# Performance work log

Hardware: AMD Instinct MI355X
Metric: run time of the kernel (lower is better)

Reference implementation:

```python
import jax, jax.numpy as jnp
import numpy as np

SCALE = 0.0625      # spatial_scale
OUT = 7             # out_size (== part_size)
C_OUT = 256         # output_dim (== input channels, group_size=1)
SPP = 4             # sample_per_part
TRANS_STD = 0.1
FC_DIM = 1024
B, H, W = 4, 128, 128
N_ROI = 2000
IMG = 2048.0        # H / SCALE


def _round_half(x):
    # CUDA round(): half away from zero (coords are non-negative here)
    return jnp.floor(x + 0.5)


def deform_roi_pool(data, rois, offset):
    """Faithful port of deform_roi_pooling (DCNv2 deform PS-ROI pooling, group_size=1).
    data: [B,C,H,W]; rois: [N,5]; offset: None or [N,2,OUT,OUT]. Returns [N,C,OUT,OUT]."""
    Bn, C, Hh, Ww = data.shape
    N = rois.shape[0]
    b = rois[:, 0].astype(jnp.int32)
    sw = _round_half(rois[:, 1]) * SCALE - 0.5
    sh = _round_half(rois[:, 2]) * SCALE - 0.5
    ew = (_round_half(rois[:, 3]) + 1.0) * SCALE - 0.5
    eh = (_round_half(rois[:, 4]) + 1.0) * SCALE - 0.5
    rw = jnp.maximum(ew - sw, 0.1)
    rh = jnp.maximum(eh - sh, 0.1)
    bw, bh = rw / OUT, rh / OUT              # bin sizes
    subw, subh = bw / SPP, bh / SPP          # sub-bin sizes

    ph, pw = jnp.meshgrid(jnp.arange(OUT, dtype=data.dtype),
                          jnp.arange(OUT, dtype=data.dtype), indexing='ij')
    wstart = pw[None] * bw[:, None, None] + sw[:, None, None]   # [N,OUT,OUT]
    hstart = ph[None] * bh[:, None, None] + sh[:, None, None]
    if offset is not None:
        # part_size == out_size -> part index == bin index
        wstart = wstart + offset[:, 0] * TRANS_STD * rw[:, None, None]
        hstart = hstart + offset[:, 1] * TRANS_STD * rh[:, None, None]

    ih2, iw2 = jnp.meshgrid(jnp.arange(SPP, dtype=data.dtype),
                            jnp.arange(SPP, dtype=data.dtype), indexing='ij')
    ih2, iw2 = ih2.reshape(-1), iw2.reshape(-1)  # [SPP*SPP]
    # sample coords [S2, N, OUT, OUT]
    ws = wstart[None] + iw2[:, None, None, None] * subw[None, :, None, None]
    hs = hstart[None] + ih2[:, None, None, None] * subh[None, :, None, None]

    bb = b[:, None, None]  # [N,1,1]

    def body(carry, coords):
        acc, cnt = carry
        w, h = coords                                 # [N,OUT,OUT]
        valid = (w >= -0.5) & (w <= Ww - 0.5) & (h >= -0.5) & (h <= Hh - 0.5)
        wc = jnp.clip(w, 0.0, Ww - 1.0)
        hc = jnp.clip(h, 0.0, Hh - 1.0)
        x0 = jnp.floor(wc).astype(jnp.int32)
        y0 = jnp.floor(hc).astype(jnp.int32)
        x1 = jnp.minimum(x0 + 1, Ww - 1)
        y1 = jnp.minimum(y0 + 1, Hh - 1)
        dx = wc - x0
        dy = hc - y0
        v00 = data[bb, :, y0, x0]   # [N,OUT,OUT,C]
        v01 = data[bb, :, y0, x1]
        v10 = data[bb, :, y1, x0]
        v11 = data[bb, :, y1, x1]
        val = (((1 - dx) * (1 - dy))[..., None] * v00
               + (dx * (1 - dy))[..., None] * v01
               + ((1 - dx) * dy)[..., None] * v10
               + (dx * dy)[..., None] * v11)
        val = jnp.where(valid[..., None], val, 0.0)
        return (acc + val, cnt + valid.astype(data.dtype)), None

    init = (jnp.zeros((N, OUT, OUT, C), data.dtype),
            jnp.zeros((N, OUT, OUT), data.dtype))
    (s, cnt), _ = jax.lax.scan(body, init, (ws, hs))
    out = jnp.where(cnt[..., None] > 0, s / jnp.maximum(cnt, 1.0)[..., None], 0.0)
    return jnp.transpose(out, (0, 3, 1, 2))  # [N,C,OUT,OUT]


def setup_inputs() -> dict:
    key = jax.random.key(0)
    ks = jax.random.split(key, 16)
    data = jax.random.normal(ks[0], (B, C_OUT, H, W), dtype=jnp.float32)
    bidx = jax.random.randint(ks[1], (N_ROI,), 0, B).astype(jnp.float32)
    x1 = jax.random.uniform(ks[2], (N_ROI,), minval=0.0, maxval=IMG - 64.0)
    y1 = jax.random.uniform(ks[3], (N_ROI,), minval=0.0, maxval=IMG - 64.0)
    wbox = jax.random.uniform(ks[4], (N_ROI,), minval=16.0, maxval=400.0)
    hbox = jax.random.uniform(ks[5], (N_ROI,), minval=16.0, maxval=400.0)
    rois = jnp.stack([bidx, x1, y1,
                      jnp.minimum(x1 + wbox, IMG - 1.0),
                      jnp.minimum(y1 + hbox, IMG - 1.0)], axis=1)
    fin = OUT * OUT * C_OUT  # 12544
    def lin(k, i, o, s=None):
        s = (1.0 / np.sqrt(i)) if s is None else s
        return jax.random.normal(k, (i, o), dtype=jnp.float32) * s
    return {
        'data': data, 'rois': rois,
        'w1': lin(ks[6], fin, FC_DIM), 'b1': jnp.zeros((FC_DIM,), jnp.float32),
        'w2': lin(ks[7], FC_DIM, FC_DIM), 'b2': jnp.zeros((FC_DIM,), jnp.float32),
        'w3': lin(ks[8], FC_DIM, OUT * OUT * 2, 0.01), 'b3': jnp.zeros((OUT * OUT * 2,), jnp.float32),
        'mw1': lin(ks[9], fin, FC_DIM), 'mb1': jnp.zeros((FC_DIM,), jnp.float32),
        'mw2': lin(ks[10], FC_DIM, OUT * OUT, 0.01), 'mb2': jnp.zeros((OUT * OUT,), jnp.float32),
    }


def reference(data, rois, w1, b1, w2, b2, w3, b3, mw1, mb1, mw2, mb2):
    n = rois.shape[0]
    x = deform_roi_pool(data, rois, None)              # [N,C,OUT,OUT]
    xf = x.reshape(n, -1)
    h = jax.nn.relu(xf @ w1 + b1)
    h = jax.nn.relu(h @ w2 + b2)
    offset = (h @ w3 + b3).reshape(n, 2, OUT, OUT)
    m = jax.nn.relu(xf @ mw1 + mb1)
    mask = jax.nn.sigmoid(m @ mw2 + mb2).reshape(n, 1, OUT, OUT)
    feat = deform_roi_pool(data, rois, offset) * mask
    return feat
```

## Files before the change

kernel.cpp:

```cpp
#include <hip/hip_runtime.h>
#include <math.h>

#define WDIM 128
#define HDIM 128
#define BDIM 4
#define CDIM 256
#define NROI 2000
#define MPAD 2048
#define FIN  12544
#define FC   1024
#define HWC  (HDIM * WDIM * CDIM)

typedef unsigned short bf16r;
typedef unsigned short u16;
typedef __attribute__((ext_vector_type(8))) short bf16x8;
typedef __attribute__((ext_vector_type(4))) float f32x4;
typedef __attribute__((ext_vector_type(8))) _Float16 half8;
typedef __attribute__((ext_vector_type(8))) unsigned short ushort8v;

__device__ __forceinline__ bf16r f2bf(float f) {
    unsigned u = __float_as_uint(f);
    u += 0x7FFFu + ((u >> 16) & 1u);
    return (bf16r)(u >> 16);
}
__device__ __forceinline__ float bf2f(bf16r h) {
    return __uint_as_float(((unsigned)h) << 16);
}
__device__ __forceinline__ u16 f2h(float f) {
    union { u16 s; _Float16 h; } c; c.h = (_Float16)f; return c.s;
}

__device__ __forceinline__ void async16(const bf16r* g, bf16r* l) {
    __builtin_amdgcn_global_load_lds(
        (const __attribute__((address_space(1))) unsigned int*)g,
        (__attribute__((address_space(3))) unsigned int*)l, 16, 0, 0);
}

#define VMW(n) asm volatile("s_waitcnt vmcnt(" #n ")" ::: "memory")
#define BARRIER() __builtin_amdgcn_s_barrier()

__device__ __forceinline__ void roi_geom(const float* __restrict__ rois, int n,
                                         int& b, float& sw, float& sh,
                                         float& rw, float& rh) {
    const float* r = rois + (size_t)n * 5;
    b = (int)r[0];
    float r1 = floorf(r[1] + 0.5f);
    float r2 = floorf(r[2] + 0.5f);
    float r3 = floorf(r[3] + 0.5f);
    float r4 = floorf(r[4] + 0.5f);
    sw = r1 * 0.0625f - 0.5f;
    sh = r2 * 0.0625f - 0.5f;
    float ew = (r3 + 1.0f) * 0.0625f - 0.5f;
    float eh = (r4 + 1.0f) * 0.0625f - 0.5f;
    rw = fmaxf(ew - sw, 0.1f);
    rh = fmaxf(eh - sh, 0.1f);
}

__device__ __forceinline__ void build_geometry(
        int n, int tid, const float* __restrict__ rois,
        const float* __restrict__ offs,
        const float* __restrict__ maskb,
        float* axW, unsigned* axMeta, uint2* wpix, int* npx, float* scale) {
    if (tid < 98) {
        int po = tid >> 1, axis = tid & 1;
        int b; float sw, sh, rw, rh;
        roi_geom(rois, n, b, sw, sh, rw, rh);
        float bw = rw * (1.f / 7.f), bh = rh * (1.f / 7.f);
        int ph = po / 7, pw = po - ph * 7;
        float start, sub;
        if (axis == 0) {
            start = (float)pw * bw + sw;
            if (offs) start += offs[(size_t)n * 98 + po] * 0.1f * rw;
            sub = bw * 0.25f;
        } else {
            start = (float)ph * bh + sh;
            if (offs) start += offs[(size_t)n * 98 + 49 + po] * 0.1f * rh;
            sub = bh * 0.25f;
        }
        float wsl[5] = {0.f, 0.f, 0.f, 0.f, 0.f};
        int base = 0, cnt = 0, mx = 0, any = 0;
#pragma unroll
        for (int i = 0; i < 4; ++i) {
            float p = start + (float)i * sub;
            bool valid = (p >= -0.5f) & (p <= 127.5f);
            float pc = fminf(fmaxf(p, 0.f), 127.f);
            int p0 = (int)floorf(pc);
            float d = pc - (float)p0;
            int p1 = min(p0 + 1, 127);
            if (valid) {
                if (!any) { base = p0; any = 1; }
                int c0 = p0 - base, c1 = p1 - base;
                float w0 = 1.f - d;
#pragma unroll
                for (int k = 0; k < 5; ++k)
                    wsl[k] += ((c0 == k) ? w0 : 0.f) + ((c1 == k) ? d : 0.f);
                cnt++;
                mx = max(mx, c1);
            }
        }
        int N = any ? mx + 1 : 0;
        axMeta[tid] = (unsigned)(N | (cnt << 3) | (base << 6));
#pragma unroll
        for (int k = 0; k < 5; ++k) axW[tid * 5 + k] = wsl[k];
    }
    __syncthreads();
    if (tid < 245) {
        int po = tid / 5, r = tid - po * 5;
        unsigned mx_ = axMeta[po * 2], my_ = axMeta[po * 2 + 1];
        int NX = mx_ & 7, NY = my_ & 7;
        int bx = (mx_ >> 6) & 127, by = (my_ >> 6) & 127;
        if (r == 0) {
            int cntx = (mx_ >> 3) & 7, cnty = (my_ >> 3) & 7;
            int ct = cntx * cnty;
            float sc = (ct > 0) ? 1.f / (float)ct : 0.f;
            if (maskb) sc *= (ct > 0) ? maskb[(size_t)n * 49 + po] : 0.f;
            npx[po] = NX * NY;
            scale[po] = sc;
        }
        if (r < NY) {
            float wyr = axW[(po * 2 + 1) * 5 + r];
            unsigned rowoff = (unsigned)(((by + r) * 128 + bx) * 512);
#pragma unroll
            for (int c = 0; c < 5; ++c)
                if (c < NX)
                    wpix[po * 28 + r * NX + c] =
                        make_uint2(rowoff + (unsigned)c * 512u,
                                   __float_as_uint(wyr * axW[po * 2 * 5 + c]));
        }
    }
    __syncthreads();
}

__device__ __forceinline__ void conv_body(const float* __restrict__ srcA,
                                          const float* __restrict__ srcB,
                                          int nsplit, int ncols, int Nout, int K,
                                          int kb, int nb, bf16r* __restrict__ dst,
                                          float (*t)[33], int tid) {
    int k0 = kb << 5, n0 = nb << 5;
    int tx = tid & 31, ty = tid >> 5;
#pragma unroll
    for (int i = 0; i < 32; i += 8) {
        int k = k0 + ty + i;
        int n = n0 + tx;
        const float* s = (n < nsplit) ? srcA : srcB;
        int col = (n < nsplit) ? n : n - nsplit;
        float v = (n < Nout && col < ncols) ? s[(size_t)k * ncols + col] : 0.f;
        t[ty + i][tx] = v;
    }
    __syncthreads();
#pragma unroll
    for (int i = 0; i < 32; i += 8) {
        int n = n0 + ty + i;
        if (n < Nout) dst[(size_t)n * K + k0 + tx] = f2bf(t[tx][ty + i]);
    }
}

__global__ __launch_bounds__(256) void prep_kernel(
        const float* __restrict__ w1, const float* __restrict__ mw1,
        const float* __restrict__ w2, const float* __restrict__ w3,
        const float* __restrict__ mw2,
        bf16r* __restrict__ bt1, bf16r* __restrict__ bt2,
        bf16r* __restrict__ bt3, bf16r* __restrict__ bt4,
        const float* __restrict__ data, u16* __restrict__ data_t) {
    __shared__ float t[32][33];
    int tid = threadIdx.x;
    int blk = blockIdx.x;
    if (blk < 25088) {
        conv_body(w1, mw1, 1024, 1024, 2048, FIN, blk % 392, blk / 392, bt1, t, tid);
        return;
    }
    blk -= 25088;
    if (blk < 1024) {
        conv_body(w2, w2, 1 << 30, 1024, 1024, 1024, blk & 31, blk >> 5, bt2, t, tid);
        return;
    }
    blk -= 1024;
    if (blk < 128) {
        conv_body(w3, w3, 1 << 30, 98, 98, 1024, blk & 31, blk >> 5, bt3, t, tid);
        return;
    }
    blk -= 128;
    if (blk < 64) {
        conv_body(mw2, mw2, 1 << 30, 49, 49, 1024, blk & 31, blk >> 5, bt4, t, tid);
        return;
    }
    blk -= 64;
    {
        int x0 = (blk & 3) << 5;
        int c0 = ((blk >> 2) & 7) << 5;
        int bz = blk >> 5;
        int b = bz >> 7, y = bz & 127;
        int tx = tid & 31, ty = tid >> 5;
#pragma unroll
        for (int i = 0; i < 32; i += 8)
            t[ty + i][tx] = data[(((size_t)b * CDIM + c0 + ty + i) * HDIM + y) * WDIM + x0 + tx];
        __syncthreads();
#pragma unroll
        for (int i = 0; i < 32; i += 8)
            data_t[(((size_t)b * HDIM + y) * WDIM + x0 + ty + i) * CDIM + c0 + tx] = f2h(t[tx][ty + i]);
    }
}

__global__ __launch_bounds__(512) void pool1_kernel(const u16* __restrict__ data_t,
                                                    const float* __restrict__ rois,
                                                    bf16r* __restrict__ xf) {
    __shared__ ushort tileX[49][264];
    __shared__ float axW[98 * 5];
    __shared__ unsigned axMeta[98];
    __shared__ uint2 wpix[49 * 28];
    __shared__ int npx[49];
    __shared__ float scale[49];
    int n = blockIdx.x, tid = threadIdx.x;
    build_geometry(n, tid, rois, nullptr, nullptr, axW, axMeta, wpix, npx, scale);
    int b = (int)rois[(size_t)n * 5];
    int wave = tid >> 6, lane = tid & 63, shalf = lane >> 5, c8 = (lane & 31) << 3;
    const char* dpb = (const char*)(data_t + (size_t)b * HWC + c8);
    for (int po = wave * 2 + shalf; po < 49; po += 16) {
        int npe = npx[po];
        float sc = scale[po];
        const uint2* wp = wpix + po * 28;
        float a[8];
#pragma unroll
        for (int k = 0; k < 8; ++k) a[k] = 0.f;
        int p = 0;
        for (; p + 2 <= npe; p += 2) {
            uint2 q0 = wp[p], q1 = wp[p + 1];
            half8 v0 = *(const half8*)(dpb + q0.x);
            half8 v1 = *(const half8*)(dpb + q1.x);
            float w0 = __uint_as_float(q0.y), w1 = __uint_as_float(q1.y);
#pragma unroll
            for (int k = 0; k < 8; ++k) a[k] += w0 * (float)v0[k];
#pragma unroll
            for (int k = 0; k < 8; ++k) a[k] += w1 * (float)v1[k];
        }
        if (p < npe) {
            uint2 q0 = wp[p];
            half8 v0 = *(const half8*)(dpb + q0.x);
            float w0 = __uint_as_float(q0.y);
#pragma unroll
            for (int k = 0; k < 8; ++k) a[k] += w0 * (float)v0[k];
        }
        ushort8v o;
#pragma unroll
        for (int k = 0; k < 8; ++k) o[k] = f2bf(a[k] * sc);
        *(ushort8v*)&tileX[po][c8] = o;
    }
    __syncthreads();
    bf16r* xp = xf + (size_t)n * FIN;
    for (int u = tid; u < 3136; u += 512) {
        int k0 = u << 2;
        ushort4 o;
#pragma unroll
        for (int j = 0; j < 4; ++j) {
            int k = k0 + j;
            int c = k / 49;
            int po = k - c * 49;
            ((ushort*)&o)[j] = tileX[po][c];
        }
        *(ushort4*)(xp + k0) = o;
    }
}

__global__ __launch_bounds__(512) void pool2_kernel(const u16* __restrict__ data_t,
                                                    const float* __restrict__ rois,
                                                    const float* __restrict__ offs,
                                                    const float* __restrict__ maskb,
                                                    float* __restrict__ out) {
    __shared__ float tile[49 * 128];
    __shared__ float axW[98 * 5];
    __shared__ unsigned axMeta[98];
    __shared__ uint2 wpix[49 * 28];
    __shared__ int npx[49];
    __shared__ float scale[49];
    int n = blockIdx.x, chalf = blockIdx.y, tid = threadIdx.x;
    build_geometry(n, tid, rois, offs, maskb, axW, axMeta, wpix, npx, scale);
    int b = (int)rois[(size_t)n * 5];
    int wave = tid >> 6, lane = tid & 63, q = lane >> 4, c8 = (lane & 15) << 3;
    const char* dpb = (const char*)(data_t + (size_t)b * HWC + chalf * 128 + c8);
    for (int po = wave * 4 + q; po < 49; po += 32) {
        int npe = npx[po];
        float sc = scale[po];
        const uint2* wp = wpix + po * 28;
        float a[8];
#pragma unroll
        for (int k = 0; k < 8; ++k) a[k] = 0.f;
        int p = 0;
        for (; p + 2 <= npe; p += 2) {
            uint2 q0 = wp[p], q1 = wp[p + 1];
            half8 v0 = *(const half8*)(dpb + q0.x);
            half8 v1 = *(const half8*)(dpb + q1.x);
            float w0 = __uint_as_float(q0.y), w1 = __uint_as_float(q1.y);
#pragma unroll
            for (int k = 0; k < 8; ++k) a[k] += w0 * (float)v0[k];
#pragma unroll
            for (int k = 0; k < 8; ++k) a[k] += w1 * (float)v1[k];
        }
        if (p < npe) {
            uint2 q0 = wp[p];
            half8 v0 = *(const half8*)(dpb + q0.x);
            float w0 = __uint_as_float(q0.y);
#pragma unroll
            for (int k = 0; k < 8; ++k) a[k] += w0 * (float)v0[k];
        }
        int cs = c8 ^ ((po & 7) << 3);
        float4 lo = make_float4(a[0] * sc, a[1] * sc, a[2] * sc, a[3] * sc);
        float4 hi = make_float4(a[4] * sc, a[5] * sc, a[6] * sc, a[7] * sc);
        *(float4*)&tile[po * 128 + cs] = lo;
        *(float4*)&tile[po * 128 + cs + 4] = hi;
    }
    __syncthreads();
    float* op = out + (size_t)n * FIN + (size_t)chalf * 6272;
    for (int i = tid; i < 6272; i += 512) {
        int c = i / 49, po = i - c * 49;
        op[i] = tile[po * 128 + (c ^ ((po & 7) << 3))];
    }
}

#define STAGE_A(buf, h, kt) do { \
    async16(Abase + (size_t)(kt) * 64 + sAoff[h][0], &lds[buf][0][((h) * 128 + wave * 8) * 64]); \
    async16(Abase + (size_t)(kt) * 64 + sAoff[h][1], &lds[buf][0][((h) * 128 + 64 + wave * 8) * 64]); \
} while (0)
#define STAGE_B(buf, h, kt) do { \
    async16(Bbase + (size_t)(kt) * 64 + sBoff[h][0], &lds[buf][1][((h) * 128 + wave * 8) * 64]); \
    async16(Bbase + (size_t)(kt) * 64 + sBoff[h][1], &lds[buf][1][((h) * 128 + 64 + wave * 8) * 64]); \
} while (0)
#define LDA_HALF(buf, mh) do { \
    const char* Ar = (const char*)&lds[buf][0][0] + aQ + (mh) * 16384; \
    _Pragma("unroll") for (int i = 0; i < 4; ++i) \
        _Pragma("unroll") for (int ks = 0; ks < 2; ++ks) \
            aF[i][ks] = *(const bf16x8*)(Ar + i * 2048 + fRB[ks]); \
} while (0)
#define LDB_HALF(dst, buf, nh) do { \
    const char* Br = (const char*)&lds[buf][1][0] + bQ + (nh) * 16384; \
    _Pragma("unroll") for (int jf = 0; jf < 2; ++jf) \
        _Pragma("unroll") for (int ks = 0; ks < 2; ++ks) \
            dst[jf][ks] = *(const bf16x8*)(Br + jf * 2048 + fRB[ks]); \
} while (0)
#define MMA_Q(mh, nh, B) do { \
    __builtin_amdgcn_s_setprio(1); \
    _Pragma("unroll") for (int i = 0; i < 4; ++i) \
        _Pragma("unroll") for (int jf = 0; jf < 2; ++jf) \
            _Pragma("unroll") for (int ks = 0; ks < 2; ++ks) \
                acc[(mh) * 4 + i][(nh) * 2 + jf] = __builtin_amdgcn_mfma_f32_16x16x32_bf16( \
                    aF[i][ks], B[jf][ks], acc[(mh) * 4 + i][(nh) * 2 + jf], 0, 0, 0); \
    __builtin_amdgcn_s_setprio(0); \
} while (0)

__global__ __launch_bounds__(512, 2) void gemm256_kernel(
        const bf16r* __restrict__ A, int lda,
        const bf16r* __restrict__ Bt, int ldb,
        bf16r* __restrict__ P, int Npad, int KS, int ktiles) {
    __shared__ bf16r lds[2][2][256 * 64];
    int tid = threadIdx.x;
    int wave = tid >> 6, lane = tid & 63;
    int l15 = lane & 15, quad = lane >> 4;
    int wm = wave >> 2, wn = wave & 3;

    int idx = blockIdx.x + gridDim.x * blockIdx.y;
    int nid = (idx & 7) * ((gridDim.x * gridDim.y) >> 3) + (idx >> 3);
    int bx = nid % gridDim.x, by = nid / gridDim.x;
    int m0 = by << 8, n0 = bx << 8;
    int z = blockIdx.z;

    int sAoff[2][2], sBoff[2][2];
#pragma unroll
    for (int h = 0; h < 2; ++h)
#pragma unroll
        for (int j = 0; j < 2; ++j) {
            int slot = h * 128 + j * 64 + wave * 8 + (lane >> 3);
            int g = (lane & 7) ^ ((slot >> 1) & 7);
            int rowA = ((slot >> 6) & 1) * 128 + (slot >> 7) * 64 + (slot & 63);
            int colB = ((slot >> 5) & 3) * 64 + (slot >> 7) * 32 + (slot & 31);
            sAoff[h][j] = rowA * lda + g * 8;
            sBoff[h][j] = colB * ldb + g * 8;
        }
    const bf16r* Abase = A + (size_t)m0 * lda;
    const bf16r* Bbase = Bt + (size_t)n0 * ldb;

    int fRB[2];
#pragma unroll
    for (int ks = 0; ks < 2; ++ks)
        fRB[ks] = l15 * 128 + ((((ks << 2) + quad) ^ ((l15 >> 1) & 7)) << 4);
    int aQ = wm * 8192;
    int bQ = wn * 4096;

    f32x4 acc[8][4];
#pragma unroll
    for (int i = 0; i < 8; ++i)
#pragma unroll
        for (int j = 0; j < 4; ++j) acc[i][j] = (f32x4){0.f, 0.f, 0.f, 0.f};
    bf16x8 aF[4][2], bF0[2][2], bF1[2][2];

    int tb = ((ktiles * z) / KS) & ~1;
    int te = (z == KS - 1) ? ktiles : ((ktiles * (z + 1)) / KS) & ~1;
    int nit = (te - tb) >> 1;

    STAGE_A(0, 0, tb); STAGE_B(0, 0, tb); STAGE_A(0, 1, tb); STAGE_B(0, 1, tb);
    STAGE_A(1, 0, tb + 1); STAGE_B(1, 0, tb + 1);
    VMW(4);
    BARRIER();

    for (int it = 0; it < nit; ++it) {
        int t1 = tb + 2 * it + 1, nx0 = t1 + 1, nx1 = t1 + 2;
        bool last = (it == nit - 1);
        LDA_HALF(0, 0); LDB_HALF(bF0, 0, 0);
        STAGE_A(1, 1, t1);
        BARRIER();
        MMA_Q(0, 0, bF0);
        BARRIER();

        LDB_HALF(bF1, 0, 1);
        STAGE_B(1, 1, t1);
        BARRIER();
        MMA_Q(0, 1, bF1);
        BARRIER();

        LDA_HALF(0, 1);
        if (!last) STAGE_A(0, 0, nx0);
        BARRIER();
        MMA_Q(1, 1, bF1);
        BARRIER();

        if (!last) STAGE_B(0, 0, nx0);
        BARRIER();
        MMA_Q(1, 0, bF0);
        if (last) { VMW(0); } else { VMW(4); }
        BARRIER();

        LDA_HALF(1, 0); LDB_HALF(bF0, 1, 0);
        if (!last) STAGE_A(0, 1, nx0);
        BARRIER();
        MMA_Q(0, 0, bF0);
        BARRIER();

        LDB_HALF(bF1, 1, 1);
        if (!last) STAGE_B(0, 1, nx0);
        BARRIER();
        MMA_Q(0, 1, bF1);
        BARRIER();

        LDA_HALF(1, 1);
        if (!last) STAGE_A(1, 0, nx1);
        BARRIER();
        MMA_Q(1, 1, bF1);
        BARRIER();

        if (!last) STAGE_B(1, 0, nx1);
        BARRIER();
        MMA_Q(1, 0, bF0);
        if (!last) { VMW(4); }
        BARRIER();
    }

    bf16r* Pp = P + (size_t)z * MPAD * Npad;
#pragma unroll
    for (int I = 0; I < 8; ++I) {
        int row = m0 + wm * 128 + I * 16 + quad * 4;
#pragma unroll
        for (int J = 0; J < 4; ++J) {
            int col = n0 + wn * 64 + J * 16 + l15;
            bf16r* o = Pp + (size_t)row * Npad + col;
#pragma unroll
            for (int r = 0; r < 4; ++r) o[(size_t)r * Npad] = f2bf(acc[I][J][r]);
        }
    }
}

__global__ __launch_bounds__(256) void gemm_mfma_kernel(
        const bf16r* __restrict__ A, int lda,
        const bf16r* __restrict__ Bt, int K,
        float* __restrict__ P, int Npad, int KS) {
    __shared__ bf16r As[128 * 32];
    __shared__ bf16r Bs[128 * 32];
    int tid = threadIdx.x;
    int wave = tid >> 6, lane = tid & 63;
    int nwgxy = gridDim.x * gridDim.y;
    int idx = blockIdx.x + gridDim.x * blockIdx.y;
    int chunk = nwgxy >> 3;
    int nid = (idx & 7) * chunk + (idx >> 3);
    int bx = nid % gridDim.x, by = nid / gridDim.x;
    int m0 = by << 7, n0 = bx << 7;
    int z = blockIdx.z;

    int srow = lane >> 2;
    int kchunk = ((lane & 3) ^ ((lane >> 3) & 3)) << 3;
    const bf16r* aG0 = A + (size_t)(m0 + wave * 32 + srow) * lda + kchunk;
    const bf16r* aG1 = A + (size_t)(m0 + wave * 32 + 16 + srow) * lda + kchunk;
    const bf16r* bG0 = Bt + (size_t)(n0 + wave * 32 + srow) * K + kchunk;
    const bf16r* bG1 = Bt + (size_t)(n0 + wave * 32 + 16 + srow) * K + kchunk;
    bf16r* aL0 = As + wave * 1024;
    bf16r* aL1 = As + wave * 1024 + 512;
    bf16r* bL0 = Bs + wave * 1024;
    bf16r* bL1 = Bs + wave * 1024 + 512;

    int l15 = lane & 15, quad = lane >> 4;
    int wr = wave >> 1, wc = wave & 1;
    int psw = (quad ^ ((l15 >> 1) & 3)) << 3;
    int aoff[4], boff[4];
#pragma unroll
    for (int t = 0; t < 4; ++t) {
        aoff[t] = ((wr * 64 + t * 16 + l15) * 32 + psw) * 2;
        boff[t] = ((wc * 64 + t * 16 + l15) * 32 + psw) * 2;
    }

    f32x4 acc[4][4];
#pragma unroll
    for (int i = 0; i < 4; ++i)
#pragma unroll
        for (int j = 0; j < 4; ++j) acc[i][j] = (f32x4){0.f, 0.f, 0.f, 0.f};

    int iters = K >> 5;
    int i0 = (int)((long)iters * z / KS);
    int i1 = (int)((long)iters * (z + 1) / KS);

    {
        size_t k0 = (size_t)i0 << 5;
        async16(aG0 + k0, aL0); async16(aG1 + k0, aL1);
        async16(bG0 + k0, bL0); async16(bG1 + k0, bL1);
    }
    for (int it = i0; it < i1; ++it) {
        __syncthreads();
        bf16x8 af[4], bfv[4];
#pragma unroll
        for (int t = 0; t < 4; ++t) af[t] = *(const bf16x8*)((const char*)As + aoff[t]);
#pragma unroll
        for (int t = 0; t < 4; ++t) bfv[t] = *(const bf16x8*)((const char*)Bs + boff[t]);
        __syncthreads();
        if (it + 1 < i1) {
            size_t k0 = (size_t)(it + 1) << 5;
            async16(aG0 + k0, aL0); async16(aG1 + k0, aL1);
            async16(bG0 + k0, bL0); async16(bG1 + k0, bL1);
        }
#pragma unroll
        for (int i = 0; i < 4; ++i)
#pragma unroll
            for (int j = 0; j < 4; ++j)
                acc[i][j] = __builtin_amdgcn_mfma_f32_16x16x32_bf16(af[i], bfv[j], acc[i][j], 0, 0, 0);
    }

    float* Pp = P + (size_t)z * MPAD * Npad;
#pragma unroll
    for (int i = 0; i < 4; ++i) {
        int row = m0 + wr * 64 + i * 16 + quad * 4;
#pragma unroll
        for (int j = 0; j < 4; ++j) {
            int col = n0 + wc * 64 + j * 16 + l15;
            float* o = Pp + (size_t)row * Npad + col;
#pragma unroll
            for (int r = 0; r < 4; ++r) o[(size_t)r * Npad] = acc[i][j][r];
        }
    }
}

__global__ __launch_bounds__(256) void gemm_tail_kernel(
        const bf16r* __restrict__ A0, int lda0,
        const bf16r* __restrict__ A1, int lda1,
        const bf16r* __restrict__ Bt0, const bf16r* __restrict__ Bt1,
        float* __restrict__ P) {
    __shared__ bf16r As[128 * 32];
    __shared__ bf16r Bs[128 * 32];
    int tid = threadIdx.x;
    int wave = tid >> 6, lane = tid & 63;
    int prob = blockIdx.y >> 4;
    int m0 = (blockIdx.y & 15) << 7;
    const bf16r* A = prob ? A1 : A0;
    int lda = prob ? lda1 : lda0;
    const bf16r* Bt = prob ? Bt1 : Bt0;
    int z = blockIdx.z;
    const int K = 1024, KS = 8, Npad = 128;

    int srow = lane >> 2;
    int kchunk = ((lane & 3) ^ ((lane >> 3) & 3)) << 3;
    const bf16r* aG0 = A + (size_t)(m0 + wave * 32 + srow) * lda + kchunk;
    const bf16r* aG1 = A + (size_t)(m0 + wave * 32 + 16 + srow) * lda + kchunk;
    const bf16r* bG0 = Bt + (size_t)(wave * 32 + srow) * K + kchunk;
    const bf16r* bG1 = Bt + (size_t)(wave * 32 + 16 + srow) * K + kchunk;
    bf16r* aL0 = As + wave * 1024;
    bf16r* aL1 = As + wave * 1024 + 512;
    bf16r* bL0 = Bs + wave * 1024;
    bf16r* bL1 = Bs + wave * 1024 + 512;

    int l15 = lane & 15, quad = lane >> 4;
    int wr = wave >> 1, wc = wave & 1;
    int psw = (quad ^ ((l15 >> 1) & 3)) << 3;
    int aoff[4], boff[4];
#pragma unroll
    for (int t = 0; t < 4; ++t) {
        aoff[t] = ((wr * 64 + t * 16 + l15) * 32 + psw) * 2;
        boff[t] = ((wc * 64 + t * 16 + l15) * 32 + psw) * 2;
    }

    f32x4 acc[4][4];
#pragma unroll
    for (int i = 0; i < 4; ++i)
#pragma unroll
        for (int j = 0; j < 4; ++j) acc[i][j] = (f32x4){0.f, 0.f, 0.f, 0.f};

    int iters = K >> 5;
    int i0 = iters * z / KS;
    int i1 = iters * (z + 1) / KS;

    {
        size_t k0 = (size_t)i0 << 5;
        async16(aG0 + k0, aL0); async16(aG1 + k0, aL1);
        async16(bG0 + k0, bL0); async16(bG1 + k0, bL1);
    }
    for (int it = i0; it < i1; ++it) {
        __syncthreads();
        bf16x8 af[4], bfv[4];
#pragma unroll
        for (int t = 0; t < 4; ++t) af[t] = *(const bf16x8*)((const char*)As + aoff[t]);
#pragma unroll
        for (int t = 0; t < 4; ++t) bfv[t] = *(const bf16x8*)((const char*)Bs + boff[t]);
        __syncthreads();
        if (it + 1 < i1) {
            size_t k0 = (size_t)(it + 1) << 5;
            async16(aG0 + k0, aL0); async16(aG1 + k0, aL1);
            async16(bG0 + k0, bL0); async16(bG1 + k0, bL1);
        }
#pragma unroll
        for (int i = 0; i < 4; ++i)
#pragma unroll
            for (int j = 0; j < 4; ++j)
                acc[i][j] = __builtin_amdgcn_mfma_f32_16x16x32_bf16(af[i], bfv[j], acc[i][j], 0, 0, 0);
    }

    float* Pp = P + (size_t)(prob * 8 + z) * (MPAD * 128);
#pragma unroll
    for (int i = 0; i < 4; ++i) {
        int row = m0 + wr * 64 + i * 16 + quad * 4;
#pragma unroll
        for (int j = 0; j < 4; ++j) {
            int col = wc * 64 + j * 16 + l15;
            float* o = Pp + (size_t)row * Npad + col;
#pragma unroll
            for (int r = 0; r < 4; ++r) o[(size_t)r * Npad] = acc[i][j][r];
        }
    }
}

__global__ __launch_bounds__(256) void reduce_kernel(
        const void* __restrict__ Pv, int shift, int KS, int pbf16,
        const float* __restrict__ bias0, const float* __restrict__ bias1, int bsplit,
        void* __restrict__ Out, int ldo, int M, int Nreal, int outmode) {
    int idx = (blockIdx.x * 256 + threadIdx.x) << 2;
    int Npad = 1 << shift;
    int row = idx >> shift, col = idx & (Npad - 1);
    f32x4 s = (f32x4){0.f, 0.f, 0.f, 0.f};
    size_t plane = (size_t)MPAD << shift;
    if (pbf16) {
        const bf16r* P = (const bf16r*)Pv;
        for (int zz = 0; zz < KS; ++zz) {
            ushort4 u = *(const ushort4*)(P + (size_t)zz * plane + idx);
            s[0] += bf2f(u.x); s[1] += bf2f(u.y); s[2] += bf2f(u.z); s[3] += bf2f(u.w);
        }
    } else {
        const float* P = (const float*)Pv;
        for (int zz = 0; zz < KS; ++zz) s += *(const f32x4*)(P + (size_t)zz * plane + idx);
    }
    if (row < M) {
#pragma unroll
        for (int e = 0; e < 4; ++e) {
            int c = col + e;
            if (c < Nreal) {
                float b = (c < bsplit) ? bias0[c] : bias1[c - bsplit];
                float v = s[e] + b;
                if (outmode == 0) {
                    v = fmaxf(v, 0.f);
                    ((bf16r*)Out)[(size_t)row * ldo + c] = f2bf(v);
                } else {
                    if (outmode == 2) v = 1.f / (1.f + expf(-v));
                    ((float*)Out)[(size_t)row * ldo + c] = v;
                }
            }
        }
    }
}

__global__ __launch_bounds__(256) void reduce34_kernel(
        const float* __restrict__ P, const float* __restrict__ b3,
        const float* __restrict__ mb2, float* __restrict__ offs,
        float* __restrict__ maskb) {
    int blk = blockIdx.x;
    int prob = blk >> 8;
    int idx = ((blk & 255) * 256 + threadIdx.x) << 2;
    int row = idx >> 7, col = idx & 127;
    f32x4 s = (f32x4){0.f, 0.f, 0.f, 0.f};
    size_t plane = (size_t)MPAD * 128;
    const float* Pb = P + (size_t)(prob * 8) * plane;
    for (int zz = 0; zz < 8; ++zz) s += *(const f32x4*)(Pb + (size_t)zz * plane + idx);
    if (row < NROI) {
        if (prob == 0) {
#pragma unroll
            for (int e = 0; e < 4; ++e) {
                int c = col + e;
                if (c < 98) offs[(size_t)row * 98 + c] = s[e] + b3[c];
            }
        } else {
#pragma unroll
            for (int e = 0; e < 4; ++e) {
                int c = col + e;
                if (c < 49) maskb[(size_t)row * 49 + c] = 1.f / (1.f + expf(-(s[e] + mb2[c])));
            }
        }
    }
}

extern "C" void kernel_launch(void* const* d_in, const int* in_sizes, int n_in,
                              void* d_out, int out_size, void* d_ws, size_t ws_size,
                              hipStream_t stream) {
    const float* data = (const float*)d_in[0];
    const float* rois = (const float*)d_in[1];
    const float* w1   = (const float*)d_in[2];
    const float* b1   = (const float*)d_in[3];
    const float* w2   = (const float*)d_in[4];
    const float* b2   = (const float*)d_in[5];
    const float* w3   = (const float*)d_in[6];
    const float* b3   = (const float*)d_in[7];
    const float* mw1  = (const float*)d_in[8];
    const float* mb1  = (const float*)d_in[9];
    const float* mw2  = (const float*)d_in[10];
    const float* mb2  = (const float*)d_in[11];
    float* out = (float*)d_out;

    char* w = (char*)d_ws;
    size_t off = 0;
    auto carve = [&](size_t bytes) {
        void* p = w + off;
        off += (bytes + 255) & ~(size_t)255;
        return p;
    };
    u16* data_t   = (u16*)carve((size_t)BDIM * HDIM * WDIM * CDIM * 2);
    bf16r* xf     = (bf16r*)carve((size_t)MPAD * FIN * 2);
    bf16r* bt1    = (bf16r*)carve((size_t)MPAD * FIN * 2);
    bf16r* hm     = (bf16r*)carve((size_t)MPAD * 2048 * 2);
    bf16r* h2     = (bf16r*)carve((size_t)MPAD * 1024 * 2);
    bf16r* bt2    = (bf16r*)carve((size_t)1024 * 1024 * 2);
    bf16r* bt3    = (bf16r*)carve((size_t)128 * 1024 * 2);
    bf16r* bt4    = (bf16r*)carve((size_t)128 * 1024 * 2);
    float* offs   = (float*)carve((size_t)NROI * 98 * 4);
    float* maskb  = (float*)carve((size_t)NROI * 49 * 4);
    void*  P      = (void*)(w + off);
    size_t plane  = (size_t)MPAD * 2048 * 4;
    size_t avail  = (ws_size > off) ? ws_size - off : 0;
    int use256 = (avail >= 4 * plane);

    prep_kernel<<<42688, 256, 0, stream>>>(w1, mw1, w2, w3, mw2,
                                           bt1, bt2, bt3, bt4, data, data_t);
    pool1_kernel<<<dim3(NROI), 512, 0, stream>>>(data_t, rois, xf);

    if (use256) {
        gemm256_kernel<<<dim3(8, 8, 4), 512, 0, stream>>>(xf, FIN, bt1, FIN,
                                                          (bf16r*)P, 2048, 4, 196);
        reduce_kernel<<<4096, 256, 0, stream>>>(P, 11, 4, 1, b1, mb1, 1024,
                                                hm, 2048, NROI, 2048, 0);
    } else {
        gemm_mfma_kernel<<<dim3(16, 16, 3), 256, 0, stream>>>(xf, FIN, bt1, FIN,
                                                              (float*)P, 2048, 3);
        reduce_kernel<<<4096, 256, 0, stream>>>(P, 11, 3, 0, b1, mb1, 1024,
                                                hm, 2048, NROI, 2048, 0);
    }
    gemm_mfma_kernel<<<dim3(8, 16, 4), 256, 0, stream>>>(hm, 2048, bt2, 1024,
                                                         (float*)P, 1024, 4);
    reduce_kernel<<<2048, 256, 0, stream>>>(P, 10, 4, 0, b2, b2, 1 << 30,
                                            h2, 1024, NROI, 1024, 0);
    gemm_tail_kernel<<<dim3(1, 32, 8), 256, 0, stream>>>(h2, 1024, hm + 1024, 2048,
                                                         bt3, bt4, (float*)P);
    reduce34_kernel<<<512, 256, 0, stream>>>((const float*)P, b3, mb2, offs, maskb);

    pool2_kernel<<<dim3(NROI, 2), 512, 0, stream>>>(data_t, rois, offs, maskb, out);
}
```

Baseline: 483.6 us.

## Drop split-K for the second and tail GEMMs and fuse bias/activation epilogues

The second FC GEMM and the offset/mask tail GEMM now run the full K loop in one workgroup each. Each writes its final activations directly: bias plus ReLU to bf16, and bias or sigmoid for the offset and mask outputs. This removes the fp32 partial-sum planes, the two reduce kernels and their launches. The cost is far fewer workgroups: 128 for the second GEMM and only 32 for the tail, each running 32 K iterations. Parallelism on a large GPU drops sharply and latency may go up for those stages. A block-index swizzle is also added to the second GEMM.

```diff
diff --git a/kernel.cpp b/kernel.cpp
--- a/kernel.cpp
+++ b/kernel.cpp
@@ -552,13 +552,96 @@
     }
 }
 
-__global__ __launch_bounds__(256) void gemm_tail_kernel(
+__global__ __launch_bounds__(256) void gemm2f_kernel(
+        const bf16r* __restrict__ A, int lda,
+        const bf16r* __restrict__ Bt,
+        const float* __restrict__ bias,
+        bf16r* __restrict__ Out) {
+    __shared__ bf16r As[128 * 32];
+    __shared__ bf16r Bs[128 * 32];
+    const int K = 1024;
+    int tid = threadIdx.x;
+    int wave = tid >> 6, lane = tid & 63;
+    int nwgxy = gridDim.x * gridDim.y;
+    int idx = blockIdx.x + gridDim.x * blockIdx.y;
+    int nid = (idx & 7) * (nwgxy >> 3) + (idx >> 3);
+    int bx = nid % gridDim.x, by = nid / gridDim.x;
+    int m0 = by << 7, n0 = bx << 7;
+
+    int srow = lane >> 2;
+    int kchunk = ((lane & 3) ^ ((lane >> 3) & 3)) << 3;
+    const bf16r* aG0 = A + (size_t)(m0 + wave * 32 + srow) * lda + kchunk;
+    const bf16r* aG1 = A + (size_t)(m0 + wave * 32 + 16 + srow) * lda + kchunk;
+    const bf16r* bG0 = Bt + (size_t)(n0 + wave * 32 + srow) * K + kchunk;
+    const bf16r* bG1 = Bt + (size_t)(n0 + wave * 32 + 16 + srow) * K + kchunk;
+    bf16r* aL0 = As + wave * 1024;
+    bf16r* aL1 = As + wave * 1024 + 512;
+    bf16r* bL0 = Bs + wave * 1024;
+    bf16r* bL1 = Bs + wave * 1024 + 512;
+
+    int l15 = lane & 15, quad = lane >> 4;
+    int wr = wave >> 1, wc = wave & 1;
+    int psw = (quad ^ ((l15 >> 1) & 3)) << 3;
+    int aoff[4], boff[4];
+#pragma unroll
+    for (int t = 0; t < 4; ++t) {
+        aoff[t] = ((wr * 64 + t * 16 + l15) * 32 + psw) * 2;
+        boff[t] = ((wc * 64 + t * 16 + l15) * 32 + psw) * 2;
+    }
+
+    f32x4 acc[4][4];
+#pragma unroll
+    for (int i = 0; i < 4; ++i)
+#pragma unroll
+        for (int j = 0; j < 4; ++j) acc[i][j] = (f32x4){0.f, 0.f, 0.f, 0.f};
+
+    {
+        async16(aG0, aL0); async16(aG1, aL1);
+        async16(bG0, bL0); async16(bG1, bL1);
+    }
+    for (int it = 0; it < 32; ++it) {
+        __syncthreads();
+        bf16x8 af[4], bfv[4];
+#pragma unroll
+        for (int t = 0; t < 4; ++t) af[t] = *(const bf16x8*)((const char*)As + aoff[t]);
+#pragma unroll
+        for (int t = 0; t < 4; ++t) bfv[t] = *(const bf16x8*)((const char*)Bs + boff[t]);
+        __syncthreads();
+        if (it + 1 < 32) {
+            size_t k0 = (size_t)(it + 1) << 5;
+            async16(aG0 + k0, aL0); async16(aG1 + k0, aL1);
+            async16(bG0 + k0, bL0); async16(bG1 + k0, bL1);
+        }
+#pragma unroll
+        for (int i = 0; i < 4; ++i)
+#pragma unroll
+            for (int j = 0; j < 4; ++j)
+                acc[i][j] = __builtin_amdgcn_mfma_f32_16x16x32_bf16(af[i], bfv[j], acc[i][j], 0, 0, 0);
+    }
+
+#pragma unroll
+    for (int i = 0; i < 4; ++i) {
+        int row = m0 + wr * 64 + i * 16 + quad * 4;
+#pragma unroll
+        for (int j = 0; j < 4; ++j) {
+            int col = n0 + wc * 64 + j * 16 + l15;
+            float b = bias[col];
+#pragma unroll
+            for (int r = 0; r < 4; ++r)
+                Out[(size_t)(row + r) * 1024 + col] = f2bf(fmaxf(acc[i][j][r] + b, 0.f));
+        }
+    }
+}
+
+__global__ __launch_bounds__(256) void tailf_kernel(
         const bf16r* __restrict__ A0, int lda0,
         const bf16r* __restrict__ A1, int lda1,
         const bf16r* __restrict__ Bt0, const bf16r* __restrict__ Bt1,
-        float* __restrict__ P) {
+        const float* __restrict__ b3, const float* __restrict__ mb2,
+        float* __restrict__ offs, float* __restrict__ maskb) {
     __shared__ bf16r As[128 * 32];
     __shared__ bf16r Bs[128 * 32];
+    const int K = 1024;
     int tid = threadIdx.x;
     int wave = tid >> 6, lane = tid & 63;
     int prob = blockIdx.y >> 4;
@@ -566,8 +649,6 @@
     const bf16r* A = prob ? A1 : A0;
     int lda = prob ? lda1 : lda0;
     const bf16r* Bt = prob ? Bt1 : Bt0;
-    int z = blockIdx.z;
-    const int K = 1024, KS = 8, Npad = 128;
 
     int srow = lane >> 2;
     int kchunk = ((lane & 3) ^ ((lane >> 3) & 3)) << 3;
@@ -596,16 +677,11 @@
 #pragma unroll
         for (int j = 0; j < 4; ++j) acc[i][j] = (f32x4){0.f, 0.f, 0.f, 0.f};
 
-    int iters = K >> 5;
-    int i0 = iters * z / KS;
-    int i1 = iters * (z + 1) / KS;
-
     {
-        size_t k0 = (size_t)i0 << 5;
-        async16(aG0 + k0, aL0); async16(aG1 + k0, aL1);
-        async16(bG0 + k0, bL0); async16(bG1 + k0, bL1);
-    }
-    for (int it = i0; it < i1; ++it) {
+        async16(aG0, aL0); async16(aG1, aL1);
+        async16(bG0, bL0); async16(bG1, bL1);
+    }
+    for (int it = 0; it < 32; ++it) {
         __syncthreads();
         bf16x8 af[4], bfv[4];
 #pragma unroll
@@ -613,7 +689,7 @@
 #pragma unroll
         for (int t = 0; t < 4; ++t) bfv[t] = *(const bf16x8*)((const char*)Bs + boff[t]);
         __syncthreads();
-        if (it + 1 < i1) {
+        if (it + 1 < 32) {
             size_t k0 = (size_t)(it + 1) << 5;
             async16(aG0 + k0, aL0); async16(aG1 + k0, aL1);
             async16(bG0 + k0, bL0); async16(bG1 + k0, bL1);
@@ -625,16 +701,25 @@
                 acc[i][j] = __builtin_amdgcn_mfma_f32_16x16x32_bf16(af[i], bfv[j], acc[i][j], 0, 0, 0);
     }
 
-    float* Pp = P + (size_t)(prob * 8 + z) * (MPAD * 128);
 #pragma unroll
     for (int i = 0; i < 4; ++i) {
         int row = m0 + wr * 64 + i * 16 + quad * 4;
 #pragma unroll
         for (int j = 0; j < 4; ++j) {
             int col = wc * 64 + j * 16 + l15;
-            float* o = Pp + (size_t)row * Npad + col;
-#pragma unroll
-            for (int r = 0; r < 4; ++r) o[(size_t)r * Npad] = acc[i][j][r];
+#pragma unroll
+            for (int r = 0; r < 4; ++r) {
+                int rr = row + r;
+                if (rr < NROI) {
+                    if (prob == 0) {
+                        if (col < 98) offs[(size_t)rr * 98 + col] = acc[i][j][r] + b3[col];
+                    } else {
+                        if (col < 49)
+                            maskb[(size_t)rr * 49 + col] =
+                                1.f / (1.f + expf(-(acc[i][j][r] + mb2[col])));
+                    }
+                }
+            }
         }
     }
 }
@@ -672,35 +757,6 @@
                     if (outmode == 2) v = 1.f / (1.f + expf(-v));
                     ((float*)Out)[(size_t)row * ldo + c] = v;
                 }
-            }
-        }
-    }
-}
-
-__global__ __launch_bounds__(256) void reduce34_kernel(
-        const float* __restrict__ P, const float* __restrict__ b3,
-        const float* __restrict__ mb2, float* __restrict__ offs,
-        float* __restrict__ maskb) {
-    int blk = blockIdx.x;
-    int prob = blk >> 8;
-    int idx = ((blk & 255) * 256 + threadIdx.x) << 2;
-    int row = idx >> 7, col = idx & 127;
-    f32x4 s = (f32x4){0.f, 0.f, 0.f, 0.f};
-    size_t plane = (size_t)MPAD * 128;
-    const float* Pb = P + (size_t)(prob * 8) * plane;
-    for (int zz = 0; zz < 8; ++zz) s += *(const f32x4*)(Pb + (size_t)zz * plane + idx);
-    if (row < NROI) {
-        if (prob == 0) {
-#pragma unroll
-            for (int e = 0; e < 4; ++e) {
-                int c = col + e;
-                if (c < 98) offs[(size_t)row * 98 + c] = s[e] + b3[c];
-            }
-        } else {
-#pragma unroll
-            for (int e = 0; e < 4; ++e) {
-                int c = col + e;
-                if (c < 49) maskb[(size_t)row * 49 + c] = 1.f / (1.f + expf(-(s[e] + mb2[c])));
             }
         }
     }
@@ -760,13 +816,9 @@
         reduce_kernel<<<4096, 256, 0, stream>>>(P, 11, 3, 0, b1, mb1, 1024,
                                                 hm, 2048, NROI, 2048, 0);
     }
-    gemm_mfma_kernel<<<dim3(8, 16, 4), 256, 0, stream>>>(hm, 2048, bt2, 1024,
-                                                         (float*)P, 1024, 4);
-    reduce_kernel<<<2048, 256, 0, stream>>>(P, 10, 4, 0, b2, b2, 1 << 30,
-                                            h2, 1024, NROI, 1024, 0);
-    gemm_tail_kernel<<<dim3(1, 32, 8), 256, 0, stream>>>(h2, 1024, hm + 1024, 2048,
-                                                         bt3, bt4, (float*)P);
-    reduce34_kernel<<<512, 256, 0, stream>>>((const float*)P, b3, mb2, offs, maskb);
+    gemm2f_kernel<<<dim3(8, 16), 256, 0, stream>>>(hm, 2048, bt2, b2, h2);
+    tailf_kernel<<<dim3(1, 32), 256, 0, stream>>>(h2, 1024, hm + 1024, 2048,
+                                                  bt3, bt4, b3, mb2, offs, maskb);
 
     pool2_kernel<<<dim3(NROI, 2), 512, 0, stream>>>(data_t, rois, offs, maskb, out);
 }
```

New measurement: 506.4 us. 1.05x slower.
